# Optimization experiments

Measured on AMD Instinct MI355X. Metric: run time of the kernel, lower is better.

## Reference

```python
import jax, jax.numpy as jnp
import numpy as np

BATCH = 2048
OBS_DIM = 48
H0, H1, H2 = 512, 256, 128
ACT_DIM = 12
NUM_TEACHERS = 64


def setup_inputs() -> dict:
    key = jax.random.key(0)
    ks = jax.random.split(key, 10)
    s = lambda fan_in: 1.0 / np.sqrt(fan_in)
    return {
        "obs": jax.random.normal(ks[0], (BATCH, OBS_DIM), dtype=jnp.float32),
        "teacher_indices": jax.random.randint(ks[1], (BATCH,), 0, NUM_TEACHERS),
        "w0": jax.random.normal(ks[2], (NUM_TEACHERS, H0, OBS_DIM), dtype=jnp.float32) * s(OBS_DIM),
        "b0": jax.random.normal(ks[3], (NUM_TEACHERS, H0), dtype=jnp.float32) * s(OBS_DIM),
        "w2": jax.random.normal(ks[4], (NUM_TEACHERS, H1, H0), dtype=jnp.float32) * s(H0),
        "b2": jax.random.normal(ks[5], (NUM_TEACHERS, H1), dtype=jnp.float32) * s(H0),
        "w4": jax.random.normal(ks[6], (NUM_TEACHERS, H2, H1), dtype=jnp.float32) * s(H1),
        "b4": jax.random.normal(ks[7], (NUM_TEACHERS, H2), dtype=jnp.float32) * s(H1),
        "w6": jax.random.normal(ks[8], (NUM_TEACHERS, ACT_DIM, H2), dtype=jnp.float32) * s(H2),
        "b6": jax.random.normal(ks[9], (NUM_TEACHERS, ACT_DIM), dtype=jnp.float32) * s(H2),
    }


def reference(obs, teacher_indices, w0, b0, w2, b2, w4, b4, w6, b6):
    # Per-sample gather of full teacher layer weights, then batched GEMV.
    def layer(x, w, b):
        # x: [B, in]; w[idx]: [B, out, in]; b[idx]: [B, out]
        return jnp.einsum("boi,bi->bo", w[teacher_indices], x) + b[teacher_indices]

    x = jax.nn.elu(layer(obs, w0, b0))
    x = jax.nn.elu(layer(x, w2, b2))
    x = jax.nn.elu(layer(x, w4, b4))
    x = jnp.tanh(layer(x, w6, b6))
    return x
```

## Files before the change

### kernel.cpp

```cpp
#include <hip/hip_runtime.h>

#define BATCH 2048
#define NTEACH 64

typedef __attribute__((ext_vector_type(8))) short short8;
typedef __attribute__((ext_vector_type(4))) float f32x4;

__device__ __forceinline__ unsigned short f2bf(float f) {
    unsigned u = __float_as_uint(f);
    u += 0x7FFFu + ((u >> 16) & 1u);
    return (unsigned short)(u >> 16);
}

__device__ __forceinline__ short8 cvt8(float4 a, float4 b) {
    short8 r;
    r[0] = (short)f2bf(a.x); r[1] = (short)f2bf(a.y);
    r[2] = (short)f2bf(a.z); r[3] = (short)f2bf(a.w);
    r[4] = (short)f2bf(b.x); r[5] = (short)f2bf(b.y);
    r[6] = (short)f2bf(b.z); r[7] = (short)f2bf(b.w);
    return r;
}

__global__ __launch_bounds__(256) void sort_kernel(const int* __restrict__ tidx,
                                                   int* __restrict__ offsets,
                                                   int* __restrict__ order) {
    __shared__ int cnt[NTEACH];
    __shared__ int offs[NTEACH + 1];
    __shared__ int cur[NTEACH];
    int tid = threadIdx.x;
    if (tid < NTEACH) cnt[tid] = 0;
    __syncthreads();
    for (int i = tid; i < BATCH; i += 256) atomicAdd(&cnt[tidx[i]], 1);
    __syncthreads();
    if (tid == 0) {
        int a = 0;
        for (int t = 0; t < NTEACH; ++t) { offs[t] = a; a += cnt[t]; }
        offs[NTEACH] = a;
    }
    __syncthreads();
    if (tid < NTEACH) cur[tid] = offs[tid];
    if (tid < NTEACH + 1) offsets[tid] = offs[tid];
    __syncthreads();
    for (int i = tid; i < BATCH; i += 256) {
        int p = atomicAdd(&cur[tidx[i]], 1);
        order[p] = i;
    }
}

__global__ __launch_bounds__(256) void gather_kernel(const float* __restrict__ obs,
                                                     const int* __restrict__ order,
                                                     unsigned short* __restrict__ obs_s) {
    int gtid = blockIdx.x * 256 + threadIdx.x;
    int r = gtid >> 3;
    int c0 = (gtid & 7) * 8;
    short8 v = {0, 0, 0, 0, 0, 0, 0, 0};
    if (c0 < 48) {
        const float* src = obs + (size_t)order[r] * 48 + c0;
        float4 a = *reinterpret_cast<const float4*>(src);
        float4 b = *reinterpret_cast<const float4*>(src + 4);
        v = cvt8(a, b);
    }
    *reinterpret_cast<short8*>(&obs_s[(size_t)r * 64 + c0]) = v;
}

template <int K, int KVALID, int NOUT>
__global__ __launch_bounds__(256) void layer_mfma(const unsigned short* __restrict__ xs,
                                                  const float* __restrict__ W,
                                                  const float* __restrict__ Bv,
                                                  const int* __restrict__ offsets,
                                                  unsigned short* __restrict__ ys) {
    constexpr int KT = K / 32;
    const int t = blockIdx.y;
    const int start = offsets[t];
    const int end = offsets[t + 1];
    if (start >= end) return;
    const int w = threadIdx.x >> 6;
    const int l = threadIdx.x & 63;
    const int ln = l & 15;
    const int kg = l >> 4;
    const int n0 = blockIdx.x * 64 + w * 16;

    short8 bfrag[KT];
    const float* wrow = W + ((size_t)t * NOUT + n0 + ln) * KVALID;
#pragma unroll
    for (int kt = 0; kt < KT; ++kt) {
        int kb = kt * 32 + kg * 8;
        short8 f = {0, 0, 0, 0, 0, 0, 0, 0};
        if (kb < KVALID) {
            float4 a = *reinterpret_cast<const float4*>(wrow + kb);
            float4 b = *reinterpret_cast<const float4*>(wrow + kb + 4);
            f = cvt8(a, b);
        }
        bfrag[kt] = f;
    }
    const float bias = Bv[(size_t)t * NOUT + n0 + ln];

    for (int r0 = start; r0 < end; r0 += 16) {
        f32x4 acc = {0.f, 0.f, 0.f, 0.f};
        const unsigned short* xrow = xs + (size_t)(r0 + ln) * K + kg * 8;
#pragma unroll
        for (int kt = 0; kt < KT; ++kt) {
            short8 af = *reinterpret_cast<const short8*>(xrow + kt * 32);
            acc = __builtin_amdgcn_mfma_f32_16x16x32_bf16(af, bfrag[kt], acc, 0, 0, 0);
        }
#pragma unroll
        for (int j = 0; j < 4; ++j) {
            int m = kg * 4 + j;
            if (r0 + m < end) {
                float v = acc[j] + bias;
                v = v > 0.f ? v : expm1f(v);
                ys[(size_t)(r0 + m) * NOUT + n0 + ln] = f2bf(v);
            }
        }
    }
}

__global__ __launch_bounds__(256) void final_mfma(const unsigned short* __restrict__ xs,
                                                  const float* __restrict__ W,
                                                  const float* __restrict__ Bv,
                                                  const int* __restrict__ offsets,
                                                  const int* __restrict__ order,
                                                  float* __restrict__ out) {
    constexpr int K = 128, KT = 4, NOUT = 12;
    const int t = blockIdx.x;
    const int start = offsets[t];
    const int end = offsets[t + 1];
    const int w = threadIdx.x >> 6;
    const int l = threadIdx.x & 63;
    const int ln = l & 15;
    const int kg = l >> 4;
    const bool nvalid = ln < NOUT;

    short8 bfrag[KT];
    const float* wrow = W + ((size_t)t * NOUT + (nvalid ? ln : 0)) * K;
#pragma unroll
    for (int kt = 0; kt < KT; ++kt) {
        int kb = kt * 32 + kg * 8;
        float4 a = *reinterpret_cast<const float4*>(wrow + kb);
        float4 b = *reinterpret_cast<const float4*>(wrow + kb + 4);
        bfrag[kt] = cvt8(a, b);
    }
    const float bias = nvalid ? Bv[(size_t)t * NOUT + ln] : 0.f;

    for (int mt = w;; mt += 4) {
        int r0 = start + mt * 16;
        if (r0 >= end) break;
        f32x4 acc = {0.f, 0.f, 0.f, 0.f};
        const unsigned short* xrow = xs + (size_t)(r0 + ln) * K + kg * 8;
#pragma unroll
        for (int kt = 0; kt < KT; ++kt) {
            short8 af = *reinterpret_cast<const short8*>(xrow + kt * 32);
            acc = __builtin_amdgcn_mfma_f32_16x16x32_bf16(af, bfrag[kt], acc, 0, 0, 0);
        }
        if (nvalid) {
#pragma unroll
            for (int j = 0; j < 4; ++j) {
                int m = kg * 4 + j;
                if (r0 + m < end)
                    out[(size_t)order[r0 + m] * NOUT + ln] = tanhf(acc[j] + bias);
            }
        }
    }
}

extern "C" void kernel_launch(void* const* d_in, const int* in_sizes, int n_in,
                              void* d_out, int out_size, void* d_ws, size_t ws_size,
                              hipStream_t stream) {
    const float* obs = (const float*)d_in[0];
    const int* tidx  = (const int*)d_in[1];
    const float* w0  = (const float*)d_in[2];
    const float* b0  = (const float*)d_in[3];
    const float* w2  = (const float*)d_in[4];
    const float* b2  = (const float*)d_in[5];
    const float* w4  = (const float*)d_in[6];
    const float* b4  = (const float*)d_in[7];
    const float* w6  = (const float*)d_in[8];
    const float* b6  = (const float*)d_in[9];
    float* out = (float*)d_out;

    const int ROWS = BATCH + 16;
    char* ws = (char*)d_ws;
    int* offsets = (int*)ws;
    int* order   = (int*)(ws + 1024);
    unsigned short* obs_s = (unsigned short*)(ws + 16384);
    unsigned short* h0 = obs_s + (size_t)ROWS * 64;
    unsigned short* h1 = h0 + (size_t)ROWS * 512;
    unsigned short* h2 = h1 + (size_t)ROWS * 256;

    sort_kernel<<<1, 256, 0, stream>>>(tidx, offsets, order);
    gather_kernel<<<64, 256, 0, stream>>>(obs, order, obs_s);
    layer_mfma<64, 48, 512><<<dim3(8, NTEACH), 256, 0, stream>>>(obs_s, w0, b0, offsets, h0);
    layer_mfma<512, 512, 256><<<dim3(4, NTEACH), 256, 0, stream>>>(h0, w2, b2, offsets, h1);
    layer_mfma<256, 256, 128><<<dim3(2, NTEACH), 256, 0, stream>>>(h1, w4, b4, offsets, h2);
    final_mfma<<<NTEACH, 256, 0, stream>>>(h2, w6, b6, offsets, order, out);
}
```

Measured before the change: 48.08 us.

## Fuse sort, gather and all four MLP layers into one per-teacher kernel

Replaces the six-kernel pipeline (sort, gather, three hidden layers, final layer) with a single kernel. Each block handles one teacher and 32-row chunks, finds its rows with ballot-based compaction, and keeps activations in swizzled LDS between layers. This removes the launch overhead and the global round-trips of the intermediate activations. In exchange, each chunk reloads and reconverts all of its teacher's weights, teachers with more than 128 rows loop serially over chunks, and every block scans the full teacher index array.

```diff
diff --git a/kernel.cpp b/kernel.cpp
--- a/kernel.cpp
+++ b/kernel.cpp
@@ -21,143 +21,200 @@
     return r;
 }
 
-__global__ __launch_bounds__(256) void sort_kernel(const int* __restrict__ tidx,
-                                                   int* __restrict__ offsets,
-                                                   int* __restrict__ order) {
-    __shared__ int cnt[NTEACH];
-    __shared__ int offs[NTEACH + 1];
-    __shared__ int cur[NTEACH];
-    int tid = threadIdx.x;
-    if (tid < NTEACH) cnt[tid] = 0;
-    __syncthreads();
-    for (int i = tid; i < BATCH; i += 256) atomicAdd(&cnt[tidx[i]], 1);
-    __syncthreads();
-    if (tid == 0) {
-        int a = 0;
-        for (int t = 0; t < NTEACH; ++t) { offs[t] = a; a += cnt[t]; }
-        offs[NTEACH] = a;
-    }
-    __syncthreads();
-    if (tid < NTEACH) cur[tid] = offs[tid];
-    if (tid < NTEACH + 1) offsets[tid] = offs[tid];
-    __syncthreads();
-    for (int i = tid; i < BATCH; i += 256) {
-        int p = atomicAdd(&cur[tidx[i]], 1);
-        order[p] = i;
-    }
-}
-
-__global__ __launch_bounds__(256) void gather_kernel(const float* __restrict__ obs,
-                                                     const int* __restrict__ order,
-                                                     unsigned short* __restrict__ obs_s) {
-    int gtid = blockIdx.x * 256 + threadIdx.x;
-    int r = gtid >> 3;
-    int c0 = (gtid & 7) * 8;
-    short8 v = {0, 0, 0, 0, 0, 0, 0, 0};
-    if (c0 < 48) {
-        const float* src = obs + (size_t)order[r] * 48 + c0;
-        float4 a = *reinterpret_cast<const float4*>(src);
-        float4 b = *reinterpret_cast<const float4*>(src + 4);
-        v = cvt8(a, b);
-    }
-    *reinterpret_cast<short8*>(&obs_s[(size_t)r * 64 + c0]) = v;
-}
-
-template <int K, int KVALID, int NOUT>
-__global__ __launch_bounds__(256) void layer_mfma(const unsigned short* __restrict__ xs,
-                                                  const float* __restrict__ W,
-                                                  const float* __restrict__ Bv,
-                                                  const int* __restrict__ offsets,
-                                                  unsigned short* __restrict__ ys) {
-    constexpr int KT = K / 32;
-    const int t = blockIdx.y;
-    const int start = offsets[t];
-    const int end = offsets[t + 1];
-    if (start >= end) return;
-    const int w = threadIdx.x >> 6;
-    const int l = threadIdx.x & 63;
-    const int ln = l & 15;
-    const int kg = l >> 4;
-    const int n0 = blockIdx.x * 64 + w * 16;
-
-    short8 bfrag[KT];
-    const float* wrow = W + ((size_t)t * NOUT + n0 + ln) * KVALID;
-#pragma unroll
-    for (int kt = 0; kt < KT; ++kt) {
-        int kb = kt * 32 + kg * 8;
-        short8 f = {0, 0, 0, 0, 0, 0, 0, 0};
-        if (kb < KVALID) {
-            float4 a = *reinterpret_cast<const float4*>(wrow + kb);
-            float4 b = *reinterpret_cast<const float4*>(wrow + kb + 4);
-            f = cvt8(a, b);
-        }
-        bfrag[kt] = f;
-    }
-    const float bias = Bv[(size_t)t * NOUT + n0 + ln];
-
-    for (int r0 = start; r0 < end; r0 += 16) {
-        f32x4 acc = {0.f, 0.f, 0.f, 0.f};
-        const unsigned short* xrow = xs + (size_t)(r0 + ln) * K + kg * 8;
-#pragma unroll
-        for (int kt = 0; kt < KT; ++kt) {
-            short8 af = *reinterpret_cast<const short8*>(xrow + kt * 32);
-            acc = __builtin_amdgcn_mfma_f32_16x16x32_bf16(af, bfrag[kt], acc, 0, 0, 0);
-        }
-#pragma unroll
-        for (int j = 0; j < 4; ++j) {
-            int m = kg * 4 + j;
-            if (r0 + m < end) {
+__global__ __launch_bounds__(1024) void fused_mlp(
+    const float* __restrict__ obs, const int* __restrict__ tidx,
+    const float* __restrict__ w0, const float* __restrict__ b0,
+    const float* __restrict__ w2, const float* __restrict__ b2,
+    const float* __restrict__ w4, const float* __restrict__ b4,
+    const float* __restrict__ w6, const float* __restrict__ b6,
+    float* __restrict__ out) {
+    __shared__ char hbuf[57344];
+    __shared__ int wsum[16];
+    __shared__ int ordc[32];
+
+    char* h0b = hbuf;
+    char* h1b = hbuf + 32768;
+    char* h2b = hbuf + 49152;
+
+    const int t = blockIdx.x;
+    const int tid = threadIdx.x;
+    const int lane = tid & 63;
+    const int wid = tid >> 6;
+    const int ln = lane & 15;
+    const int kg = lane >> 4;
+
+    for (int c = blockIdx.y;; c += gridDim.y) {
+        const int cbase = c * 32;
+        __syncthreads();
+        int carry = 0;
+#pragma unroll
+        for (int r = 0; r < 2; ++r) {
+            int i = r * 1024 + tid;
+            bool f = (tidx[i] == t);
+            unsigned long long b = __ballot(f);
+            if (lane == 0) wsum[wid] = __builtin_popcountll(b);
+            int below = __builtin_popcountll(b & ((1ull << lane) - 1ull));
+            __syncthreads();
+            int wbase = 0, tot = 0;
+#pragma unroll
+            for (int j = 0; j < 16; ++j) {
+                int s = wsum[j];
+                if (j < wid) wbase += s;
+                tot += s;
+            }
+            int rank = carry + wbase + below;
+            if (f && rank >= cbase && rank < cbase + 32) ordc[rank - cbase] = i;
+            carry += tot;
+            __syncthreads();
+        }
+        const int count = carry;
+        if (cbase >= count) break;
+        const int nv = min(32, count - cbase);
+
+        {
+            const int n0 = wid * 32;
+            short8 bf[2][2];
+#pragma unroll
+            for (int nt = 0; nt < 2; ++nt) {
+                const float* wr = w0 + ((size_t)t * 512 + n0 + nt * 16 + ln) * 48;
+#pragma unroll
+                for (int kt = 0; kt < 2; ++kt) {
+                    int kb = kt * 32 + kg * 8;
+                    short8 f8 = {0, 0, 0, 0, 0, 0, 0, 0};
+                    if (kb < 48)
+                        f8 = cvt8(*(const float4*)(wr + kb), *(const float4*)(wr + kb + 4));
+                    bf[nt][kt] = f8;
+                }
+            }
+#pragma unroll
+            for (int mt = 0; mt < 2; ++mt) {
+                int lr = mt * 16 + ln;
+                int arow = (lr < nv) ? ordc[lr] : ordc[0];
+                const float* xr = obs + (size_t)arow * 48;
+                short8 af[2];
+#pragma unroll
+                for (int kt = 0; kt < 2; ++kt) {
+                    int kb = kt * 32 + kg * 8;
+                    short8 f8 = {0, 0, 0, 0, 0, 0, 0, 0};
+                    if (kb < 48)
+                        f8 = cvt8(*(const float4*)(xr + kb), *(const float4*)(xr + kb + 4));
+                    af[kt] = f8;
+                }
+#pragma unroll
+                for (int nt = 0; nt < 2; ++nt) {
+                    f32x4 acc = {0.f, 0.f, 0.f, 0.f};
+                    acc = __builtin_amdgcn_mfma_f32_16x16x32_bf16(af[0], bf[nt][0], acc, 0, 0, 0);
+                    acc = __builtin_amdgcn_mfma_f32_16x16x32_bf16(af[1], bf[nt][1], acc, 0, 0, 0);
+                    int col = n0 + nt * 16 + ln;
+                    float bias = b0[(size_t)t * 512 + col];
+#pragma unroll
+                    for (int j = 0; j < 4; ++j) {
+                        int row = mt * 16 + kg * 4 + j;
+                        float v = acc[j] + bias;
+                        v = v > 0.f ? v : expm1f(v);
+                        int byte = (row * 1024 + col * 2) ^ ((row & 7) << 4);
+                        *(unsigned short*)(h0b + byte) = f2bf(v);
+                    }
+                }
+            }
+        }
+        __syncthreads();
+
+        {
+            const int n0 = wid * 16;
+            f32x4 acc[2] = {{0.f, 0.f, 0.f, 0.f}, {0.f, 0.f, 0.f, 0.f}};
+#pragma unroll
+            for (int kh = 0; kh < 2; ++kh) {
+                short8 bf[8];
+                const float* wr = w2 + ((size_t)t * 256 + n0 + ln) * 512 + kh * 256;
+#pragma unroll
+                for (int k8 = 0; k8 < 8; ++k8) {
+                    int kb = k8 * 32 + kg * 8;
+                    bf[k8] = cvt8(*(const float4*)(wr + kb), *(const float4*)(wr + kb + 4));
+                }
+#pragma unroll
+                for (int mt = 0; mt < 2; ++mt) {
+                    int row = mt * 16 + ln;
+#pragma unroll
+                    for (int k8 = 0; k8 < 8; ++k8) {
+                        int col0 = kh * 256 + k8 * 32 + kg * 8;
+                        int byte = (row * 1024 + col0 * 2) ^ ((row & 7) << 4);
+                        short8 af = *(const short8*)(h0b + byte);
+                        acc[mt] = __builtin_amdgcn_mfma_f32_16x16x32_bf16(af, bf[k8], acc[mt], 0, 0, 0);
+                    }
+                }
+            }
+            int col = n0 + ln;
+            float bias = b2[(size_t)t * 256 + col];
+#pragma unroll
+            for (int mt = 0; mt < 2; ++mt)
+#pragma unroll
+                for (int j = 0; j < 4; ++j) {
+                    int row = mt * 16 + kg * 4 + j;
+                    float v = acc[mt][j] + bias;
+                    v = v > 0.f ? v : expm1f(v);
+                    int byte = (row * 512 + col * 2) ^ ((row & 7) << 4);
+                    *(unsigned short*)(h1b + byte) = f2bf(v);
+                }
+        }
+        __syncthreads();
+
+        {
+            const int nt = wid & 7, mt = wid >> 3;
+            const int n0 = nt * 16;
+            short8 bf[8];
+            const float* wr = w4 + ((size_t)t * 128 + n0 + ln) * 256;
+#pragma unroll
+            for (int k8 = 0; k8 < 8; ++k8) {
+                int kb = k8 * 32 + kg * 8;
+                bf[k8] = cvt8(*(const float4*)(wr + kb), *(const float4*)(wr + kb + 4));
+            }
+            f32x4 acc = {0.f, 0.f, 0.f, 0.f};
+            int row = mt * 16 + ln;
+#pragma unroll
+            for (int k8 = 0; k8 < 8; ++k8) {
+                int col0 = k8 * 32 + kg * 8;
+                int byte = (row * 512 + col0 * 2) ^ ((row & 7) << 4);
+                short8 af = *(const short8*)(h1b + byte);
+                acc = __builtin_amdgcn_mfma_f32_16x16x32_bf16(af, bf[k8], acc, 0, 0, 0);
+            }
+            int col = n0 + ln;
+            float bias = b4[(size_t)t * 128 + col];
+#pragma unroll
+            for (int j = 0; j < 4; ++j) {
+                int orow = mt * 16 + kg * 4 + j;
                 float v = acc[j] + bias;
                 v = v > 0.f ? v : expm1f(v);
-                ys[(size_t)(r0 + m) * NOUT + n0 + ln] = f2bf(v);
-            }
-        }
-    }
-}
-
-__global__ __launch_bounds__(256) void final_mfma(const unsigned short* __restrict__ xs,
-                                                  const float* __restrict__ W,
-                                                  const float* __restrict__ Bv,
-                                                  const int* __restrict__ offsets,
-                                                  const int* __restrict__ order,
-                                                  float* __restrict__ out) {
-    constexpr int K = 128, KT = 4, NOUT = 12;
-    const int t = blockIdx.x;
-    const int start = offsets[t];
-    const int end = offsets[t + 1];
-    const int w = threadIdx.x >> 6;
-    const int l = threadIdx.x & 63;
-    const int ln = l & 15;
-    const int kg = l >> 4;
-    const bool nvalid = ln < NOUT;
-
-    short8 bfrag[KT];
-    const float* wrow = W + ((size_t)t * NOUT + (nvalid ? ln : 0)) * K;
-#pragma unroll
-    for (int kt = 0; kt < KT; ++kt) {
-        int kb = kt * 32 + kg * 8;
-        float4 a = *reinterpret_cast<const float4*>(wrow + kb);
-        float4 b = *reinterpret_cast<const float4*>(wrow + kb + 4);
-        bfrag[kt] = cvt8(a, b);
-    }
-    const float bias = nvalid ? Bv[(size_t)t * NOUT + ln] : 0.f;
-
-    for (int mt = w;; mt += 4) {
-        int r0 = start + mt * 16;
-        if (r0 >= end) break;
-        f32x4 acc = {0.f, 0.f, 0.f, 0.f};
-        const unsigned short* xrow = xs + (size_t)(r0 + ln) * K + kg * 8;
-#pragma unroll
-        for (int kt = 0; kt < KT; ++kt) {
-            short8 af = *reinterpret_cast<const short8*>(xrow + kt * 32);
-            acc = __builtin_amdgcn_mfma_f32_16x16x32_bf16(af, bfrag[kt], acc, 0, 0, 0);
-        }
-        if (nvalid) {
+                int byte = (orow * 256 + col * 2) ^ ((orow & 7) << 4);
+                *(unsigned short*)(h2b + byte) = f2bf(v);
+            }
+        }
+        __syncthreads();
+
+        if (wid < 2) {
+            const int mt = wid;
+            short8 bf[4];
+            const float* wr = w6 + ((size_t)t * 12 + (ln < 12 ? ln : 0)) * 128;
+#pragma unroll
+            for (int kt = 0; kt < 4; ++kt) {
+                int kb = kt * 32 + kg * 8;
+                bf[kt] = cvt8(*(const float4*)(wr + kb), *(const float4*)(wr + kb + 4));
+            }
+            f32x4 acc = {0.f, 0.f, 0.f, 0.f};
+            int row = mt * 16 + ln;
+#pragma unroll
+            for (int kt = 0; kt < 4; ++kt) {
+                int col0 = kt * 32 + kg * 8;
+                int byte = (row * 256 + col0 * 2) ^ ((row & 7) << 4);
+                short8 af = *(const short8*)(h2b + byte);
+                acc = __builtin_amdgcn_mfma_f32_16x16x32_bf16(af, bf[kt], acc, 0, 0, 0);
+            }
+            float bias = (ln < 12) ? b6[(size_t)t * 12 + ln] : 0.f;
 #pragma unroll
             for (int j = 0; j < 4; ++j) {
-                int m = kg * 4 + j;
-                if (r0 + m < end)
-                    out[(size_t)order[r0 + m] * NOUT + ln] = tanhf(acc[j] + bias);
+                int orow = mt * 16 + kg * 4 + j;
+                if (ln < 12 && cbase + orow < count)
+                    out[(size_t)ordc[orow] * 12 + ln] = tanhf(acc[j] + bias);
             }
         }
     }
@@ -178,19 +235,6 @@
     const float* b6  = (const float*)d_in[9];
     float* out = (float*)d_out;
 
-    const int ROWS = BATCH + 16;
-    char* ws = (char*)d_ws;
-    int* offsets = (int*)ws;
-    int* order   = (int*)(ws + 1024);
-    unsigned short* obs_s = (unsigned short*)(ws + 16384);
-    unsigned short* h0 = obs_s + (size_t)ROWS * 64;
-    unsigned short* h1 = h0 + (size_t)ROWS * 512;
-    unsigned short* h2 = h1 + (size_t)ROWS * 256;
-
-    sort_kernel<<<1, 256, 0, stream>>>(tidx, offsets, order);
-    gather_kernel<<<64, 256, 0, stream>>>(obs, order, obs_s);
-    layer_mfma<64, 48, 512><<<dim3(8, NTEACH), 256, 0, stream>>>(obs_s, w0, b0, offsets, h0);
-    layer_mfma<512, 512, 256><<<dim3(4, NTEACH), 256, 0, stream>>>(h0, w2, b2, offsets, h1);
-    layer_mfma<256, 256, 128><<<dim3(2, NTEACH), 256, 0, stream>>>(h1, w4, b4, offsets, h2);
-    final_mfma<<<NTEACH, 256, 0, stream>>>(h2, w6, b6, offsets, order, out);
-}
+    fused_mlp<<<dim3(NTEACH, 4), 1024, 0, stream>>>(obs, tidx, w0, b0, w2, b2,
+                                                    w4, b4, w6, b6, out);
+}
```

Result: slower. 59.44 us (+23.6%).
